# Kernel optimization log

Hardware: AMD Instinct MI355X
Metric: run time of the kernel (lower is better)

The kernel has to match this reference:

```python
import jax, jax.numpy as jnp
import numpy as np

K = 16  # top-k neighbors (init kwarg k)
EPS = 1e-8


def setup_inputs() -> dict:
    key = jax.random.key(0)
    # bs=8, closeness=12, flows=2, N=2048
    x_c = jax.random.normal(key, (8, 12, 2, 2048), dtype=jnp.float32)
    return {"x_c": x_c, "flow": 0}


def _cosine_adjacency(x):
    # x: (bs, 2, N, closeness) -> per-node feature = concat of both flows over time
    bs, f, N, c = x.shape
    feats = jnp.transpose(x, (0, 2, 1, 3)).reshape(bs, N, f * c)  # (bs, N, 2*closeness)
    fn = feats / (jnp.linalg.norm(feats, axis=-1, keepdims=True) + EPS)
    return jnp.einsum('bnd,bmd->bnm', fn, fn)  # (bs, N, N)


def reference(x_c, flow):
    # x_c: (bs, closeness, 2, N)
    bs, closeness, _, N = x_c.shape
    x = jnp.transpose(x_c, (0, 2, 3, 1)).astype(jnp.float32)  # (bs, 2, N, closeness)

    # mode == 'cos': cosine-similarity adjacency
    A = _cosine_adjacency(x)

    # index = argsort(A, descending)[:, :, :k]  ==  top-k neighbor indices per node
    _, index = jax.lax.top_k(A, K)  # (bs, N, K)

    # batched gather replacing the bs x N python double loop:
    # sx_c[i, j] = x[i, flow, index[i, j]]
    x_flow = x[:, flow]  # (bs, N, closeness)
    sx_c = jax.vmap(lambda xf, idx: xf[idx])(x_flow, index)  # (bs, N, K, closeness)

    # tgt_mode == 'c': tgt = x[:, flow].unsqueeze(-2)  -> (bs, N, 1, closeness)
    tgt = x_flow[:, :, None, :]
    # returned as tgt.permute(0,2,3,1).squeeze(1) -> (bs, closeness, N)
    tgt_out = jnp.squeeze(jnp.transpose(tgt, (0, 2, 3, 1)), axis=1)

    return sx_c, tgt_out
```

## Files before the change

### kernel.cpp

```cpp
#include <hip/hip_runtime.h>
#include <hip/hip_bf16.h>
#include <math.h>

#define BS   8
#define NPTS 2048
#define CCH  12
#define NF   2
#define DIM  24
#define KPAD 32
#define KTOP 16
#define NWV  16
#define CBUF 112
#define CBS  113
#define RS   72

#define NROWS    (BS * NPTS)
#define TGT_BASE (NROWS * KTOP * CCH)

typedef unsigned long long u64;
typedef unsigned int       u32;
typedef unsigned short     u16;
typedef __attribute__((ext_vector_type(8))) short short8;
typedef __attribute__((ext_vector_type(4))) float f32x4;

#define WS_FEATS 0
#define WS_RAW   (NROWS * DIM * 4)
#define WS_FHI   (WS_RAW + NROWS * CCH * 4)
#define WS_FLO   (WS_FHI + NROWS * KPAD * 2)

__device__ __forceinline__ float np_norm_den(const float* __restrict__ v)
{
#pragma clang fp contract(off)
    float s[DIM];
    #pragma unroll
    for (int d = 0; d < DIM; ++d) s[d] = v[d] * v[d];
    float r[8];
    #pragma unroll
    for (int j = 0; j < 8; ++j) r[j] = (s[j] + s[j + 8]) + s[j + 16];
    float res = ((r[0] + r[1]) + (r[2] + r[3])) + ((r[4] + r[5]) + (r[6] + r[7]));
    return sqrtf(res) + 1e-8f;
}

__device__ __forceinline__ u32 ordf(float f)
{
    u32 u = __float_as_uint(f);
    return ((int)u >= 0) ? (u | 0x80000000u) : ~u;
}

__device__ __forceinline__ u16 bf16_rne(float x)
{
    u32 bits = __float_as_uint(x);
    bits += 0x7fffu + ((bits >> 16) & 1u);
    return (u16)(bits >> 16);
}

__global__ __launch_bounds__(256) void prep_kernel(
    const float* __restrict__ x_c,
    const int*   __restrict__ flow_p,
    float*       __restrict__ feats,
    u16*         __restrict__ fhi,
    u16*         __restrict__ flo,
    float*       __restrict__ raw,
    float*       __restrict__ out)
{
    const int t = blockIdx.x * 256 + threadIdx.x;
    const int b = t >> 11;
    const int n = t & (NPTS - 1);
    const float* xb = x_c + (size_t)b * CCH * NF * NPTS;

    float v[DIM];
    float fn[DIM];
    {
#pragma clang fp contract(off)
        #pragma unroll
        for (int c = 0; c < CCH; ++c)
            #pragma unroll
            for (int f = 0; f < NF; ++f)
                v[f * CCH + c] = xb[(c * NF + f) * NPTS + n];

        const float den = np_norm_den(v);
        float* fo = feats + (size_t)t * DIM;
        #pragma unroll
        for (int d = 0; d < DIM; ++d) { fn[d] = v[d] / den; fo[d] = fn[d]; }
    }

    u16* ho = fhi + (size_t)t * KPAD;
    u16* lo = flo + (size_t)t * KPAD;
    #pragma unroll
    for (int d = 0; d < DIM; ++d) {
        const u16 hb = bf16_rne(fn[d]);
        const float hf = __uint_as_float((u32)hb << 16);
        ho[d] = hb;
        lo[d] = bf16_rne(fn[d] - hf);
    }
    #pragma unroll
    for (int d = DIM; d < KPAD; ++d) { ho[d] = 0; lo[d] = 0; }

    const int flow = flow_p[0];
    float* ro = raw + (size_t)t * CCH;
    #pragma unroll
    for (int c = 0; c < CCH; ++c) {
        const float xv = flow ? v[CCH + c] : v[c];
        ro[c] = xv;
        out[TGT_BASE + ((size_t)b * CCH + c) * NPTS + n] = xv;
    }
}

__global__ __launch_bounds__(1024) void fused_topk_kernel(
    const float* __restrict__ feats,
    const u16*   __restrict__ fhi,
    const u16*   __restrict__ flo,
    const float* __restrict__ raw,
    float*       __restrict__ out)
{
    __shared__ union {
        float cval[NWV * 16 * RS];
        u64   ckey[64 * CBS];
    } sh;
    __shared__ float thr_s[64];
    __shared__ int   cnt[64];
    __shared__ int   sel[64][KTOP];

    const int tid  = threadIdx.x;
    const int lane = tid & 63;
    const int w    = __builtin_amdgcn_readfirstlane(tid >> 6);
    const int b     = blockIdx.x >> 5;
    const int chunk = blockIdx.x & 31;
    const int rb    = chunk * 64;
    const int p     = lane & 15;
    const int q     = lane >> 4;

    if (tid < 64) cnt[tid] = 0;

    short8 ahi[4], alo[4];
    #pragma unroll
    for (int m = 0; m < 4; ++m) {
        const size_t ae = ((size_t)(b * NPTS + rb + m * 16 + p)) * KPAD + q * 8;
        ahi[m] = *(const short8*)(fhi + ae);
        alo[m] = *(const short8*)(flo + ae);
    }

    float* wval = sh.cval + w * (16 * RS);

    float vlist[KTOP];
    #pragma unroll
    for (int k = 0; k < KTOP; ++k) vlist[k] = -3.0f;

    {
        size_t be_n = ((size_t)(b * NPTS + w * 64 + p)) * KPAD + q * 8;
        short8 nbhi = *(const short8*)(fhi + be_n);
        short8 nblo = *(const short8*)(flo + be_n);
        for (int t = 0; t < 4; ++t) {
            const int cb0 = w * 64 + t * 16;
            const short8 bhi = nbhi, blo = nblo;
            if (t < 3) {
                const size_t be = ((size_t)(b * NPTS + cb0 + 16 + p)) * KPAD + q * 8;
                nbhi = *(const short8*)(fhi + be);
                nblo = *(const short8*)(flo + be);
            }
            #pragma unroll
            for (int m = 0; m < 4; ++m) {
                f32x4 acc = {0.0f, 0.0f, 0.0f, 0.0f};
                acc = __builtin_amdgcn_mfma_f32_16x16x32_bf16(ahi[m], bhi, acc, 0, 0, 0);
                acc = __builtin_amdgcn_mfma_f32_16x16x32_bf16(ahi[m], blo, acc, 0, 0, 0);
                acc = __builtin_amdgcn_mfma_f32_16x16x32_bf16(alo[m], bhi, acc, 0, 0, 0);
                *(f32x4*)(wval + p * RS + m * 16 + q * 4) = acc;
            }
            float bv[16];
            #pragma unroll
            for (int j = 0; j < 16; ++j) bv[j] = wval[j * RS + lane];
            #pragma unroll
            for (int k = 2; k <= 16; k <<= 1)
                #pragma unroll
                for (int j = k >> 1; j > 0; j >>= 1)
                    #pragma unroll
                    for (int i = 0; i < 16; ++i) {
                        const int l = i | j;
                        if (l > i) {
                            const float a = bv[i], c = bv[l];
                            if ((i & k) == 0) { bv[i] = fminf(a, c); bv[l] = fmaxf(a, c); }
                            else              { bv[i] = fmaxf(a, c); bv[l] = fminf(a, c); }
                        }
                    }
            #pragma unroll
            for (int i = 0; i < 16; ++i) vlist[i] = fmaxf(vlist[i], bv[i]);
            #pragma unroll
            for (int j = 8; j > 0; j >>= 1)
                #pragma unroll
                for (int i = 0; i < 16; ++i) {
                    const int l = i | j;
                    if (l > i) {
                        const float a = vlist[i], c = vlist[l];
                        vlist[i] = fmaxf(a, c);
                        vlist[l] = fminf(a, c);
                    }
                }
        }
    }

    __syncthreads();

    float* vk = sh.cval;
    for (int half = NWV / 2; half >= 1; half >>= 1) {
        if (w >= half && w < 2 * half) {
            #pragma unroll
            for (int k = 0; k < KTOP; ++k)
                vk[(w * KTOP + k) * 64 + lane] = vlist[k];
        }
        __syncthreads();
        if (w < half) {
            float other[KTOP];
            #pragma unroll
            for (int k = 0; k < KTOP; ++k)
                other[k] = vk[((w + half) * KTOP + k) * 64 + lane];
            #pragma unroll
            for (int i = 0; i < KTOP; ++i)
                vlist[i] = fmaxf(vlist[i], other[KTOP - 1 - i]);
            #pragma unroll
            for (int j = 8; j > 0; j >>= 1)
                #pragma unroll
                for (int i = 0; i < KTOP; ++i) {
                    const int l = i | j;
                    if (l > i) {
                        const float a = vlist[i], c = vlist[l];
                        vlist[i] = fmaxf(a, c);
                        vlist[l] = fminf(a, c);
                    }
                }
        }
        __syncthreads();
    }
    if (w == 0) thr_s[lane] = vlist[KTOP - 1] - 8e-4f;
    __syncthreads();

    float thrv[4][4];
    #pragma unroll
    for (int m = 0; m < 4; ++m)
        #pragma unroll
        for (int i = 0; i < 4; ++i)
            thrv[m][i] = thr_s[m * 16 + q * 4 + i];

    {
        size_t be_n = ((size_t)(b * NPTS + w * 128 + p)) * KPAD + q * 8;
        short8 nbhi = *(const short8*)(fhi + be_n);
        short8 nblo = *(const short8*)(flo + be_n);
        for (int t = 0; t < 8; ++t) {
            const int cb0 = w * 128 + t * 16;
            const short8 bhi = nbhi, blo = nblo;
            if (t < 7) {
                const size_t be = ((size_t)(b * NPTS + cb0 + 16 + p)) * KPAD + q * 8;
                nbhi = *(const short8*)(fhi + be);
                nblo = *(const short8*)(flo + be);
            }
            #pragma unroll
            for (int m = 0; m < 4; ++m) {
                f32x4 acc = {0.0f, 0.0f, 0.0f, 0.0f};
                acc = __builtin_amdgcn_mfma_f32_16x16x32_bf16(ahi[m], bhi, acc, 0, 0, 0);
                acc = __builtin_amdgcn_mfma_f32_16x16x32_bf16(ahi[m], blo, acc, 0, 0, 0);
                acc = __builtin_amdgcn_mfma_f32_16x16x32_bf16(alo[m], bhi, acc, 0, 0, 0);
                #pragma unroll
                for (int i = 0; i < 4; ++i) {
                    if (acc[i] >= thrv[m][i]) {
                        const int r = m * 16 + q * 4 + i;
                        const int pos = atomicAdd(&cnt[r], 1);
                        if (pos < CBUF)
                            sh.ckey[r * CBS + pos] = (u64)(u32)(cb0 + p);
                    }
                }
            }
        }
    }
    __syncthreads();

    {
        const float* fr = feats + (size_t)(b * NPTS + rb + lane) * DIM;
        float rfn[DIM];
        #pragma unroll
        for (int d = 0; d < DIM; ++d) rfn[d] = fr[d];
        const int e = (cnt[lane] < CBUF) ? cnt[lane] : CBUF;
        for (int pos = w; pos < e; pos += NWV) {
            const int idx = (int)(u32)sh.ckey[lane * CBS + pos];
            const float* cp = feats + (size_t)(b * NPTS + idx) * DIM;
            float acc = 0.0f;
            #pragma unroll
            for (int d = 0; d < DIM; ++d)
                acc = __builtin_fmaf(cp[d], rfn[d], acc);
            sh.ckey[lane * CBS + pos] = ((u64)ordf(acc) << 32) | (u32)(2047 - idx);
        }
    }
    __syncthreads();

    {
        const int L = tid >> 4;
        const int g = tid & 15;
        const int e = (cnt[L] < CBUF) ? cnt[L] : CBUF;
        const u64* rowbuf = &sh.ckey[L * CBS];
        for (int pos = g; pos < e; pos += 16) {
            const u64 key = rowbuf[pos];
            int rank = 0;
            for (int p2 = 0; p2 < e; ++p2) rank += (rowbuf[p2] > key);
            if (rank < KTOP) sel[L][rank] = 2047 - (int)(key & 0xFFFFFFFFull);
        }
    }
    __syncthreads();

    const int rg = b * NPTS + rb;
    for (int e = tid; e < 64 * KTOP * CCH; e += 1024) {
        const int L = e / (KTOP * CCH);
        const int r = e % (KTOP * CCH);
        const int k = r / CCH;
        const int c = r % CCH;
        out[((size_t)(rg + L) * KTOP + k) * CCH + c] =
            raw[((size_t)b * NPTS + sel[L][k]) * CCH + c];
    }
}

extern "C" void kernel_launch(void* const* d_in, const int* in_sizes, int n_in,
                              void* d_out, int out_size, void* d_ws, size_t ws_size,
                              hipStream_t stream)
{
    const float* x_c    = (const float*)d_in[0];
    const int*   flow_p = (const int*)d_in[1];
    float*       out    = (float*)d_out;

    float* feats = (float*)((char*)d_ws + WS_FEATS);
    float* raw   = (float*)((char*)d_ws + WS_RAW);
    u16*   fhi   = (u16*)  ((char*)d_ws + WS_FHI);
    u16*   flo   = (u16*)  ((char*)d_ws + WS_FLO);

    prep_kernel<<<NROWS / 256, 256, 0, stream>>>(x_c, flow_p, feats, fhi, flo, raw, out);
    fused_topk_kernel<<<BS * 32, 1024, 0, stream>>>(feats, fhi, flo, raw, out);
}
```

Baseline: 105.4 us.

## Shrink top-k blocks to 16 rows and 8 waves, merge lists via shuffles

Each block now handles 16 query rows with 8 waves instead of 64 rows with 16 waves, and the grid grows from 256 to 1024 blocks. The goal is to use more CUs on the 256-CU device and to cut per-block shared-memory and barrier cost. The threshold pass samples 1024 of the 2048 columns as before, now split as 128 per wave, and the per-lane partial lists are first merged across the four lane groups with xor shuffles before the shared-memory reduction tree. The trade-off is that each block re-reads all B-operand columns for only 16 rows, so MFMA work per global load falls and total L2 traffic on fhi/flo rises about fourfold.

```diff
diff --git a/kernel.cpp b/kernel.cpp
--- a/kernel.cpp
+++ b/kernel.cpp
@@ -9,10 +9,11 @@
 #define DIM  24
 #define KPAD 32
 #define KTOP 16
-#define NWV  16
+#define NWV  8
+#define RPB  16
 #define CBUF 112
 #define CBS  113
-#define RS   72
+#define WVS  20
 
 #define NROWS    (BS * NPTS)
 #define TGT_BASE (NROWS * KTOP * CCH)
@@ -106,7 +107,20 @@
     }
 }
 
-__global__ __launch_bounds__(1024) void fused_topk_kernel(
+#define CLEANUP_DESC(arr)                                         \
+    _Pragma("unroll")                                             \
+    for (int j_ = 8; j_ > 0; j_ >>= 1)                            \
+        _Pragma("unroll")                                         \
+        for (int i_ = 0; i_ < KTOP; ++i_) {                       \
+            const int l_ = i_ | j_;                               \
+            if (l_ > i_) {                                        \
+                const float a_ = arr[i_], c_ = arr[l_];           \
+                arr[i_] = fmaxf(a_, c_);                          \
+                arr[l_] = fminf(a_, c_);                          \
+            }                                                     \
+        }
+
+__global__ __launch_bounds__(512) void fused_topk_kernel(
     const float* __restrict__ feats,
     const u16*   __restrict__ fhi,
     const u16*   __restrict__ flo,
@@ -114,158 +128,135 @@
     float*       __restrict__ out)
 {
     __shared__ union {
-        float cval[NWV * 16 * RS];
-        u64   ckey[64 * CBS];
+        float wval[NWV * 16 * WVS];
+        float vk[NWV * KTOP * 16];
+        u64   ckey[RPB * CBS];
     } sh;
-    __shared__ float thr_s[64];
-    __shared__ int   cnt[64];
-    __shared__ int   sel[64][KTOP];
+    __shared__ float thr_s[RPB];
+    __shared__ int   cnt[RPB];
+    __shared__ int   sel[RPB][KTOP];
 
     const int tid  = threadIdx.x;
     const int lane = tid & 63;
     const int w    = __builtin_amdgcn_readfirstlane(tid >> 6);
-    const int b     = blockIdx.x >> 5;
-    const int chunk = blockIdx.x & 31;
-    const int rb    = chunk * 64;
+    const int b     = blockIdx.x >> 7;
+    const int chunk = blockIdx.x & 127;
+    const int rb    = chunk * RPB;
     const int p     = lane & 15;
     const int q     = lane >> 4;
 
-    if (tid < 64) cnt[tid] = 0;
-
-    short8 ahi[4], alo[4];
-    #pragma unroll
-    for (int m = 0; m < 4; ++m) {
-        const size_t ae = ((size_t)(b * NPTS + rb + m * 16 + p)) * KPAD + q * 8;
-        ahi[m] = *(const short8*)(fhi + ae);
-        alo[m] = *(const short8*)(flo + ae);
-    }
-
-    float* wval = sh.cval + w * (16 * RS);
+    if (tid < RPB) cnt[tid] = 0;
+
+    short8 ahi, alo;
+    {
+        const size_t ae = ((size_t)(b * NPTS + rb + p)) * KPAD + q * 8;
+        ahi = *(const short8*)(fhi + ae);
+        alo = *(const short8*)(flo + ae);
+    }
+
+    float* wv = sh.wval + w * (16 * WVS);
 
     float vlist[KTOP];
     #pragma unroll
     for (int k = 0; k < KTOP; ++k) vlist[k] = -3.0f;
 
-    {
-        size_t be_n = ((size_t)(b * NPTS + w * 64 + p)) * KPAD + q * 8;
+    for (int ro = 0; ro < 2; ++ro) {
+        float bv[16];
+        #pragma unroll
+        for (int t = 0; t < 4; ++t) {
+            const int cb0 = w * 128 + ro * 64 + t * 16;
+            const size_t be = ((size_t)(b * NPTS + cb0 + p)) * KPAD + q * 8;
+            const short8 bhi = *(const short8*)(fhi + be);
+            const short8 blo = *(const short8*)(flo + be);
+            f32x4 acc = {0.0f, 0.0f, 0.0f, 0.0f};
+            acc = __builtin_amdgcn_mfma_f32_16x16x32_bf16(ahi, bhi, acc, 0, 0, 0);
+            acc = __builtin_amdgcn_mfma_f32_16x16x32_bf16(ahi, blo, acc, 0, 0, 0);
+            acc = __builtin_amdgcn_mfma_f32_16x16x32_bf16(alo, bhi, acc, 0, 0, 0);
+            *(f32x4*)(wv + p * WVS + q * 4) = acc;
+            #pragma unroll
+            for (int i = 0; i < 4; ++i)
+                bv[t * 4 + i] = wv[(q * 4 + i) * WVS + p];
+        }
+        #pragma unroll
+        for (int k = 2; k <= 16; k <<= 1)
+            #pragma unroll
+            for (int j = k >> 1; j > 0; j >>= 1)
+                #pragma unroll
+                for (int i = 0; i < 16; ++i) {
+                    const int l = i | j;
+                    if (l > i) {
+                        const float a = bv[i], c = bv[l];
+                        if ((i & k) == 0) { bv[i] = fminf(a, c); bv[l] = fmaxf(a, c); }
+                        else              { bv[i] = fmaxf(a, c); bv[l] = fminf(a, c); }
+                    }
+                }
+        #pragma unroll
+        for (int i = 0; i < 16; ++i) vlist[i] = fmaxf(vlist[i], bv[i]);
+        CLEANUP_DESC(vlist)
+    }
+
+    #pragma unroll
+    for (int x = 16; x <= 32; x <<= 1) {
+        float other[KTOP];
+        #pragma unroll
+        for (int k = 0; k < KTOP; ++k) other[k] = __shfl_xor(vlist[k], x);
+        #pragma unroll
+        for (int i = 0; i < KTOP; ++i)
+            vlist[i] = fmaxf(vlist[i], other[KTOP - 1 - i]);
+        CLEANUP_DESC(vlist)
+    }
+
+    __syncthreads();
+
+    for (int half = NWV / 2; half >= 1; half >>= 1) {
+        if (w >= half && w < 2 * half && q == 0) {
+            #pragma unroll
+            for (int k = 0; k < KTOP; ++k)
+                sh.vk[(w * KTOP + k) * 16 + p] = vlist[k];
+        }
+        __syncthreads();
+        if (w < half) {
+            float other[KTOP];
+            #pragma unroll
+            for (int k = 0; k < KTOP; ++k)
+                other[k] = sh.vk[((w + half) * KTOP + k) * 16 + p];
+            #pragma unroll
+            for (int i = 0; i < KTOP; ++i)
+                vlist[i] = fmaxf(vlist[i], other[KTOP - 1 - i]);
+            CLEANUP_DESC(vlist)
+        }
+        __syncthreads();
+    }
+    if (w == 0 && q == 0) thr_s[p] = vlist[KTOP - 1] - 8e-4f;
+    __syncthreads();
+
+    float thrv[4];
+    #pragma unroll
+    for (int i = 0; i < 4; ++i) thrv[i] = thr_s[q * 4 + i];
+
+    {
+        size_t be_n = ((size_t)(b * NPTS + w * 256 + p)) * KPAD + q * 8;
         short8 nbhi = *(const short8*)(fhi + be_n);
         short8 nblo = *(const short8*)(flo + be_n);
-        for (int t = 0; t < 4; ++t) {
-            const int cb0 = w * 64 + t * 16;
+        for (int t = 0; t < 16; ++t) {
+            const int cb0 = w * 256 + t * 16;
             const short8 bhi = nbhi, blo = nblo;
-            if (t < 3) {
+            if (t < 15) {
                 const size_t be = ((size_t)(b * NPTS + cb0 + 16 + p)) * KPAD + q * 8;
                 nbhi = *(const short8*)(fhi + be);
                 nblo = *(const short8*)(flo + be);
             }
-            #pragma unroll
-            for (int m = 0; m < 4; ++m) {
-                f32x4 acc = {0.0f, 0.0f, 0.0f, 0.0f};
-                acc = __builtin_amdgcn_mfma_f32_16x16x32_bf16(ahi[m], bhi, acc, 0, 0, 0);
-                acc = __builtin_amdgcn_mfma_f32_16x16x32_bf16(ahi[m], blo, acc, 0, 0, 0);
-                acc = __builtin_amdgcn_mfma_f32_16x16x32_bf16(alo[m], bhi, acc, 0, 0, 0);
-                *(f32x4*)(wval + p * RS + m * 16 + q * 4) = acc;
-            }
-            float bv[16];
-            #pragma unroll
-            for (int j = 0; j < 16; ++j) bv[j] = wval[j * RS + lane];
-            #pragma unroll
-            for (int k = 2; k <= 16; k <<= 1)
-                #pragma unroll
-                for (int j = k >> 1; j > 0; j >>= 1)
-                    #pragma unroll
-                    for (int i = 0; i < 16; ++i) {
-                        const int l = i | j;
-                        if (l > i) {
-                            const float a = bv[i], c = bv[l];
-                            if ((i & k) == 0) { bv[i] = fminf(a, c); bv[l] = fmaxf(a, c); }
-                            else              { bv[i] = fmaxf(a, c); bv[l] = fminf(a, c); }
-                        }
-                    }
-            #pragma unroll
-            for (int i = 0; i < 16; ++i) vlist[i] = fmaxf(vlist[i], bv[i]);
-            #pragma unroll
-            for (int j = 8; j > 0; j >>= 1)
-                #pragma unroll
-                for (int i = 0; i < 16; ++i) {
-                    const int l = i | j;
-                    if (l > i) {
-                        const float a = vlist[i], c = vlist[l];
-                        vlist[i] = fmaxf(a, c);
-                        vlist[l] = fminf(a, c);
-                    }
-                }
-        }
-    }
-
-    __syncthreads();
-
-    float* vk = sh.cval;
-    for (int half = NWV / 2; half >= 1; half >>= 1) {
-        if (w >= half && w < 2 * half) {
-            #pragma unroll
-            for (int k = 0; k < KTOP; ++k)
-                vk[(w * KTOP + k) * 64 + lane] = vlist[k];
-        }
-        __syncthreads();
-        if (w < half) {
-            float other[KTOP];
-            #pragma unroll
-            for (int k = 0; k < KTOP; ++k)
-                other[k] = vk[((w + half) * KTOP + k) * 64 + lane];
-            #pragma unroll
-            for (int i = 0; i < KTOP; ++i)
-                vlist[i] = fmaxf(vlist[i], other[KTOP - 1 - i]);
-            #pragma unroll
-            for (int j = 8; j > 0; j >>= 1)
-                #pragma unroll
-                for (int i = 0; i < KTOP; ++i) {
-                    const int l = i | j;
-                    if (l > i) {
-                        const float a = vlist[i], c = vlist[l];
-                        vlist[i] = fmaxf(a, c);
-                        vlist[l] = fminf(a, c);
-                    }
-                }
-        }
-        __syncthreads();
-    }
-    if (w == 0) thr_s[lane] = vlist[KTOP - 1] - 8e-4f;
-    __syncthreads();
-
-    float thrv[4][4];
-    #pragma unroll
-    for (int m = 0; m < 4; ++m)
-        #pragma unroll
-        for (int i = 0; i < 4; ++i)
-            thrv[m][i] = thr_s[m * 16 + q * 4 + i];
-
-    {
-        size_t be_n = ((size_t)(b * NPTS + w * 128 + p)) * KPAD + q * 8;
-        short8 nbhi = *(const short8*)(fhi + be_n);
-        short8 nblo = *(const short8*)(flo + be_n);
-        for (int t = 0; t < 8; ++t) {
-            const int cb0 = w * 128 + t * 16;
-            const short8 bhi = nbhi, blo = nblo;
-            if (t < 7) {
-                const size_t be = ((size_t)(b * NPTS + cb0 + 16 + p)) * KPAD + q * 8;
-                nbhi = *(const short8*)(fhi + be);
-                nblo = *(const short8*)(flo + be);
-            }
-            #pragma unroll
-            for (int m = 0; m < 4; ++m) {
-                f32x4 acc = {0.0f, 0.0f, 0.0f, 0.0f};
-                acc = __builtin_amdgcn_mfma_f32_16x16x32_bf16(ahi[m], bhi, acc, 0, 0, 0);
-                acc = __builtin_amdgcn_mfma_f32_16x16x32_bf16(ahi[m], blo, acc, 0, 0, 0);
-                acc = __builtin_amdgcn_mfma_f32_16x16x32_bf16(alo[m], bhi, acc, 0, 0, 0);
-                #pragma unroll
-                for (int i = 0; i < 4; ++i) {
-                    if (acc[i] >= thrv[m][i]) {
-                        const int r = m * 16 + q * 4 + i;
-                        const int pos = atomicAdd(&cnt[r], 1);
-                        if (pos < CBUF)
-                            sh.ckey[r * CBS + pos] = (u64)(u32)(cb0 + p);
-                    }
+            f32x4 acc = {0.0f, 0.0f, 0.0f, 0.0f};
+            acc = __builtin_amdgcn_mfma_f32_16x16x32_bf16(ahi, bhi, acc, 0, 0, 0);
+            acc = __builtin_amdgcn_mfma_f32_16x16x32_bf16(ahi, blo, acc, 0, 0, 0);
+            acc = __builtin_amdgcn_mfma_f32_16x16x32_bf16(alo, bhi, acc, 0, 0, 0);
+            #pragma unroll
+            for (int i = 0; i < 4; ++i) {
+                if (acc[i] >= thrv[i]) {
+                    const int r = q * 4 + i;
+                    const int pos = atomicAdd(&cnt[r], 1);
+                    if (pos < CBUF)
+                        sh.ckey[r * CBS + pos] = (u64)(u32)(cb0 + p);
                 }
             }
         }
@@ -273,29 +264,30 @@
     __syncthreads();
 
     {
-        const float* fr = feats + (size_t)(b * NPTS + rb + lane) * DIM;
+        const int r = tid & 15;
+        const float* fr = feats + (size_t)(b * NPTS + rb + r) * DIM;
         float rfn[DIM];
         #pragma unroll
         for (int d = 0; d < DIM; ++d) rfn[d] = fr[d];
-        const int e = (cnt[lane] < CBUF) ? cnt[lane] : CBUF;
-        for (int pos = w; pos < e; pos += NWV) {
-            const int idx = (int)(u32)sh.ckey[lane * CBS + pos];
+        const int e = (cnt[r] < CBUF) ? cnt[r] : CBUF;
+        for (int pos = tid >> 4; pos < e; pos += 32) {
+            const int idx = (int)(u32)sh.ckey[r * CBS + pos];
             const float* cp = feats + (size_t)(b * NPTS + idx) * DIM;
             float acc = 0.0f;
             #pragma unroll
             for (int d = 0; d < DIM; ++d)
                 acc = __builtin_fmaf(cp[d], rfn[d], acc);
-            sh.ckey[lane * CBS + pos] = ((u64)ordf(acc) << 32) | (u32)(2047 - idx);
-        }
-    }
-    __syncthreads();
-
-    {
-        const int L = tid >> 4;
-        const int g = tid & 15;
+            sh.ckey[r * CBS + pos] = ((u64)ordf(acc) << 32) | (u32)(2047 - idx);
+        }
+    }
+    __syncthreads();
+
+    {
+        const int L = tid >> 5;
+        const int g = tid & 31;
         const int e = (cnt[L] < CBUF) ? cnt[L] : CBUF;
         const u64* rowbuf = &sh.ckey[L * CBS];
-        for (int pos = g; pos < e; pos += 16) {
+        for (int pos = g; pos < e; pos += 32) {
             const u64 key = rowbuf[pos];
             int rank = 0;
             for (int p2 = 0; p2 < e; ++p2) rank += (rowbuf[p2] > key);
@@ -305,9 +297,9 @@
     __syncthreads();
 
     const int rg = b * NPTS + rb;
-    for (int e = tid; e < 64 * KTOP * CCH; e += 1024) {
-        const int L = e / (KTOP * CCH);
-        const int r = e % (KTOP * CCH);
+    for (int e2 = tid; e2 < RPB * KTOP * CCH; e2 += 512) {
+        const int L = e2 / (KTOP * CCH);
+        const int r = e2 % (KTOP * CCH);
         const int k = r / CCH;
         const int c = r % CCH;
         out[((size_t)(rg + L) * KTOP + k) * CCH + c] =
@@ -329,5 +321,5 @@
     u16*   flo   = (u16*)  ((char*)d_ws + WS_FLO);
 
     prep_kernel<<<NROWS / 256, 256, 0, stream>>>(x_c, flow_p, feats, fhi, flo, raw, out);
-    fused_topk_kernel<<<BS * 32, 1024, 0, stream>>>(feats, fhi, flo, raw, out);
-}
+    fused_topk_kernel<<<BS * 128, 512, 0, stream>>>(feats, fhi, flo, raw, out);
+}
```

Result: faster. 101.6 us (-3.6%).
